# Performance work log

Hardware: AMD Instinct MI355X
Metric: run time of the kernel (lower is better)

The kernel has to match this reference:

```python
import jax, jax.numpy as jnp
import numpy as np

H = 1024
HEADS = 16
FFN = 4096
EPS = 1e-5


def _layernorm(x, g, b):
    mu = jnp.mean(x, axis=-1, keepdims=True)
    var = jnp.mean((x - mu) ** 2, axis=-1, keepdims=True)
    return (x - mu) * jax.lax.rsqrt(var + EPS) * g + b


def setup_inputs() -> dict:
    key = jax.random.key(0)
    ks = jax.random.split(key, 12)
    N, L = 2, 2048
    s = 1.0 / np.sqrt(H)
    inp = {
        "src_hidden": jax.random.normal(ks[0], (N, L, H), dtype=jnp.float32),
        "key_mask": jnp.ones((N, L), dtype=jnp.int32),
        "Wq": jax.random.normal(ks[1], (H, H), dtype=jnp.float32) * s,
        "bq": jnp.zeros((H,), dtype=jnp.float32),
        "Wk": jax.random.normal(ks[2], (H, H), dtype=jnp.float32) * s,
        "bk": jnp.zeros((H,), dtype=jnp.float32),
        "Wv": jax.random.normal(ks[3], (H, H), dtype=jnp.float32) * s,
        "bv": jnp.zeros((H,), dtype=jnp.float32),
        "Wo": jax.random.normal(ks[4], (H, H), dtype=jnp.float32) * s,
        "bo": jnp.zeros((H,), dtype=jnp.float32),
        "ln1_g": jnp.ones((H,), dtype=jnp.float32),
        "ln1_b": jnp.zeros((H,), dtype=jnp.float32),
        "W1": jax.random.normal(ks[5], (H, FFN), dtype=jnp.float32) * s,
        "b1": jnp.zeros((FFN,), dtype=jnp.float32),
        "W2": jax.random.normal(ks[6], (FFN, H), dtype=jnp.float32) * (1.0 / np.sqrt(FFN)),
        "b2": jnp.zeros((H,), dtype=jnp.float32),
        "ln2_g": jnp.ones((H,), dtype=jnp.float32),
        "ln2_b": jnp.zeros((H,), dtype=jnp.float32),
    }
    return inp


def reference(src_hidden, key_mask, Wq, bq, Wk, bk, Wv, bv, Wo, bo,
              ln1_g, ln1_b, W1, b1, W2, b2, ln2_g, ln2_b):
    N, L, _ = src_hidden.shape
    d = H // HEADS
    # projections -> (N, heads, L, d)
    q = (src_hidden @ Wq + bq).reshape(N, L, HEADS, d).transpose(0, 2, 1, 3)
    k = (src_hidden @ Wk + bk).reshape(N, L, HEADS, d).transpose(0, 2, 1, 3)
    v = (src_hidden @ Wv + bv).reshape(N, L, HEADS, d).transpose(0, 2, 1, 3)
    # faithful quirk: Q/=sqrt(H) and K/=sqrt(H)  =>  scores scaled by 1/H
    sims = jnp.einsum('bhid,bhjd->bhij', q, k) / H  # (N, heads, L, L)
    mask = key_mask[:, None, None, :] != 0          # (N,1,1,L), masked=False
    sims = jnp.where(mask, sims, -jnp.inf)
    attn = jax.nn.softmax(sims, axis=-1)
    ctx = jnp.einsum('bhij,bhjd->bhid', attn, v)
    concats = ctx.transpose(0, 2, 1, 3).reshape(N, L, H)
    mhsa = concats @ Wo + bo
    # residual + LN1
    x = _layernorm(mhsa + src_hidden, ln1_g, ln1_b)
    # FFN (dropout=0 / eval) + residual + LN2
    ffn = jax.nn.relu(x @ W1 + b1) @ W2 + b2
    out = _layernorm(ffn + x, ln2_g, ln2_b)
    return out
```

## Files before the change

### kernel.cpp

```cpp
#include <hip/hip_runtime.h>
#include <math.h>

#define Hd   1024
#define SEQL 2048
#define NB   2
#define NHEADS 16
#define FFND 4096
#define ROWS 4096
#define QKVLD 3072

typedef __attribute__((ext_vector_type(8))) short short8;
typedef __attribute__((ext_vector_type(4))) float f32x4;

__device__ __forceinline__ unsigned short f2bf(float f) {
  union { float f; unsigned int u; } v; v.f = f;
  return (unsigned short)((v.u + 0x7fffu + ((v.u >> 16) & 1u)) >> 16);
}
__device__ __forceinline__ unsigned short f2bf_fast(float f) {
  union { float f; unsigned int u; } v; v.f = f;
  return (unsigned short)((v.u + 0x8000u) >> 16);
}
__device__ __forceinline__ float bf2f(unsigned short u) {
  union { unsigned int u; float f; } v; v.u = (unsigned int)u << 16;
  return v.f;
}

__device__ __forceinline__ void gl_lds16(const unsigned short* g,
                                         unsigned short* l) {
  __builtin_amdgcn_global_load_lds(
      (const __attribute__((address_space(1))) void*)g,
      (__attribute__((address_space(3))) void*)l, 16, 0, 0);
}

__global__ __launch_bounds__(256) void convert_bf16(
    const float* __restrict__ in, unsigned short* __restrict__ out) {
  const int i = (blockIdx.x * 256 + threadIdx.x) * 4;
  float4 x = *(const float4*)&in[i];
  ushort4 o;
  o.x = f2bf(x.x); o.y = f2bf(x.y); o.z = f2bf(x.z); o.w = f2bf(x.w);
  *(ushort4*)&out[i] = o;
}

__global__ __launch_bounds__(256) void convert_transpose(
    const float* __restrict__ W, int ld,
    unsigned short* __restrict__ Wt, int ldt) {
  __shared__ float T[64][65];
  const int t = threadIdx.x;
  const int c0 = blockIdx.x * 64, r0 = blockIdx.y * 64;
#pragma unroll
  for (int p = 0; p < 4; ++p) {
    const int lin = t + p * 256;
    const int r = lin >> 4, c4 = (lin & 15) * 4;
    float4 x = *(const float4*)&W[(size_t)(r0 + r) * ld + c0 + c4];
    T[r][c4 + 0] = x.x; T[r][c4 + 1] = x.y;
    T[r][c4 + 2] = x.z; T[r][c4 + 3] = x.w;
  }
  __syncthreads();
#pragma unroll
  for (int p = 0; p < 2; ++p) {
    const int lin = t + p * 256;
    const int oc = lin >> 3, ch = (lin & 7) * 8;
    union { unsigned short u[8]; uint4 v; } x;
#pragma unroll
    for (int i = 0; i < 8; ++i) x.u[i] = f2bf(T[ch + i][oc]);
    *(uint4*)&Wt[(size_t)(c0 + oc) * ldt + r0 + ch] = x.v;
  }
}

__global__ __launch_bounds__(256) void convert_transpose4(
    const float* __restrict__ W0, const float* __restrict__ W1,
    const float* __restrict__ W2, const float* __restrict__ W3,
    unsigned short* __restrict__ T0, unsigned short* __restrict__ T1,
    unsigned short* __restrict__ T2, unsigned short* __restrict__ T3) {
  __shared__ float T[64][65];
  const float* W = (blockIdx.z == 0) ? W0 : (blockIdx.z == 1) ? W1
                 : (blockIdx.z == 2) ? W2 : W3;
  unsigned short* Wt = (blockIdx.z == 0) ? T0 : (blockIdx.z == 1) ? T1
                     : (blockIdx.z == 2) ? T2 : T3;
  const int t = threadIdx.x;
  const int c0 = blockIdx.x * 64, r0 = blockIdx.y * 64;
#pragma unroll
  for (int p = 0; p < 4; ++p) {
    const int lin = t + p * 256;
    const int r = lin >> 4, c4 = (lin & 15) * 4;
    float4 x = *(const float4*)&W[(size_t)(r0 + r) * Hd + c0 + c4];
    T[r][c4 + 0] = x.x; T[r][c4 + 1] = x.y;
    T[r][c4 + 2] = x.z; T[r][c4 + 3] = x.w;
  }
  __syncthreads();
#pragma unroll
  for (int p = 0; p < 2; ++p) {
    const int lin = t + p * 256;
    const int oc = lin >> 3, ch = (lin & 7) * 8;
    union { unsigned short u[8]; uint4 v; } x;
#pragma unroll
    for (int i = 0; i < 8; ++i) x.u[i] = f2bf(T[ch + i][oc]);
    *(uint4*)&Wt[(size_t)(c0 + oc) * Hd + r0 + ch] = x.v;
  }
}

__global__ __launch_bounds__(256) void concat3(
    const float* __restrict__ a, const float* __restrict__ b,
    const float* __restrict__ c, float* __restrict__ o) {
  const int i = blockIdx.x * 256 + threadIdx.x;
  o[i] = (i < 1024) ? a[i] : (i < 2048 ? b[i - 1024] : c[i - 2048]);
}

__global__ __launch_bounds__(256) void transpose_v(
    const unsigned short* __restrict__ v, unsigned short* __restrict__ vt) {
  __shared__ unsigned short T[64][72];
  const int t = threadIdx.x;
  const int s0 = (blockIdx.x & 31) * 64;
  const int bh = blockIdx.x >> 5;
  const int b = bh >> 4, h = bh & 15;
#pragma unroll
  for (int p = 0; p < 2; ++p) {
    const int lin = t + p * 256;
    const int r = lin >> 3, c8 = (lin & 7) * 8;
    *(uint4*)&T[r][c8] =
        *(const uint4*)&v[(size_t)(b * SEQL + s0 + r) * QKVLD + h * 64 + c8];
  }
  __syncthreads();
#pragma unroll
  for (int p = 0; p < 2; ++p) {
    const int lin = t + p * 256;
    const int d = lin >> 3, c8 = (lin & 7) * 8;
    union { unsigned short u[8]; uint4 v4; } x;
#pragma unroll
    for (int i = 0; i < 8; ++i) x.u[i] = T[c8 + i][d];
    *(uint4*)&vt[(size_t)(bh * 64 + d) * SEQL + s0 + c8] = x.v4;
  }
}

template <int BN, int MODE, int OUTBF>
__global__ __launch_bounds__(256, (BN == 128 ? 3 : 4)) void gemm_bt(
    const unsigned short* __restrict__ A, int lda,
    const unsigned short* __restrict__ Bt, int ldb,
    const float* __restrict__ bias,
    void* __restrict__ Cv, int ldc, int K) {
  constexpr int NI = (BN == 128) ? 4 : 2;
  __shared__ unsigned short As[128 * 32];
  __shared__ unsigned short Bs[BN * 32];
  const int t = threadIdx.x;
  const int wave = t >> 6, lane = t & 63;
  const int l16 = lane & 15, quad = lane >> 4;
  const int m0 = blockIdx.y * 128, n0 = blockIdx.x * BN;
  const int wm = (wave >> 1) * 64, wn = (wave & 1) * (BN / 2);
  const int srow = wave * 16 + (lane >> 2);
  const int scol = (lane & 3) * 8;

  f32x4 acc[4][NI];
#pragma unroll
  for (int i = 0; i < 4; ++i)
#pragma unroll
    for (int j = 0; j < NI; ++j) acc[i][j] = (f32x4){0.f, 0.f, 0.f, 0.f};

  const unsigned short* Ap0 = &A[(size_t)(m0 + srow) * lda + scol];
  const unsigned short* Ap1 = &A[(size_t)(m0 + 64 + srow) * lda + scol];
  const unsigned short* Bp0 = &Bt[(size_t)(n0 + srow) * ldb + scol];
  const unsigned short* Bp1 =
      (BN == 128) ? &Bt[(size_t)(n0 + 64 + srow) * ldb + scol] : Bp0;
  unsigned short* lA0 = &As[(wave * 16) * 32];
  unsigned short* lA1 = &As[(64 + wave * 16) * 32];
  unsigned short* lB0 = &Bs[(wave * 16) * 32];
  unsigned short* lB1 = (BN == 128) ? &Bs[(64 + wave * 16) * 32] : lB0;

  for (int k0 = 0; k0 < K; k0 += 32) {
    gl_lds16(Ap0 + k0, lA0);
    gl_lds16(Ap1 + k0, lA1);
    gl_lds16(Bp0 + k0, lB0);
    if (BN == 128) gl_lds16(Bp1 + k0, lB1);
    __syncthreads();

    short8 af[4], bfr[NI];
#pragma unroll
    for (int mi = 0; mi < 4; ++mi)
      af[mi] = *(const short8*)&As[(wm + mi * 16 + l16) * 32 + quad * 8];
#pragma unroll
    for (int ni = 0; ni < NI; ++ni)
      bfr[ni] = *(const short8*)&Bs[(wn + ni * 16 + l16) * 32 + quad * 8];
#pragma unroll
    for (int mi = 0; mi < 4; ++mi)
#pragma unroll
      for (int ni = 0; ni < NI; ++ni)
        acc[mi][ni] = __builtin_amdgcn_mfma_f32_16x16x32_bf16(
            af[mi], bfr[ni], acc[mi][ni], 0, 0, 0);
    __syncthreads();
  }

#pragma unroll
  for (int mi = 0; mi < 4; ++mi) {
#pragma unroll
    for (int ni = 0; ni < NI; ++ni) {
      const int col = n0 + wn + ni * 16 + l16;
      const float bv = (MODE == 2) ? 0.0f : bias[col];
#pragma unroll
      for (int r = 0; r < 4; ++r) {
        const int row = m0 + wm + mi * 16 + quad * 4 + r;
        float v = acc[mi][ni][r] + bv;
        if (MODE == 1) v = fmaxf(v, 0.0f);
        if (OUTBF) {
          ((unsigned short*)Cv)[(size_t)row * ldc + col] = f2bf_fast(v);
        } else {
          float* Cf = (float*)Cv;
          if (MODE == 2) Cf[(size_t)row * ldc + col] += v;
          else           Cf[(size_t)row * ldc + col] = v;
        }
      }
    }
  }
}

template <int MODE>
__global__ __launch_bounds__(512, 2) void gemm256(
    const unsigned short* __restrict__ A, int lda,
    const unsigned short* __restrict__ Bt, int ldb,
    const float* __restrict__ bias,
    unsigned short* __restrict__ C, int ldc, int K) {
  __shared__ unsigned short As[2][256 * 64];
  __shared__ unsigned short Bs[2][256 * 64];
  const int t = threadIdx.x;
  const int wave = t >> 6, lane = t & 63;
  const int l16 = lane & 15, quad = lane >> 4;
  const int m0 = blockIdx.y * 256, n0 = blockIdx.x * 256;
  const int wm = (wave >> 2) * 128, wn = (wave & 3) * 64;

  const int srow = t >> 3;
  const int scol = 8 * ((t & 7) ^ ((t >> 3) & 7));
  const unsigned short* Ab = &A[(size_t)(m0 + srow) * lda + scol];
  const unsigned short* Bb = &Bt[(size_t)(n0 + srow) * ldb + scol];

  auto stgA = [&](int buf, int kt, int h) {
    const unsigned short* g = Ab + (size_t)(h * 128) * lda + kt * 64;
    unsigned short* l = &As[buf][h * 8192 + wave * 512];
    gl_lds16(g, l);
    gl_lds16(g + (size_t)64 * lda, l + 4096);
  };
  auto stgB = [&](int buf, int kt, int h) {
    const unsigned short* g = Bb + (size_t)(h * 128) * ldb + kt * 64;
    unsigned short* l = &Bs[buf][h * 8192 + wave * 512];
    gl_lds16(g, l);
    gl_lds16(g + (size_t)64 * ldb, l + 4096);
  };

  f32x4 acc[8][4];
#pragma unroll
  for (int i = 0; i < 8; ++i)
#pragma unroll
    for (int j = 0; j < 4; ++j) acc[i][j] = (f32x4){0.f, 0.f, 0.f, 0.f};

  const int NT = K >> 6;

  stgA(0, 0, 0); stgA(0, 0, 1);
  stgB(0, 0, 0); stgB(0, 0, 1);
  if (NT > 1) {
    stgB(1, 1, 0); stgB(1, 1, 1);
    asm volatile("s_waitcnt vmcnt(4)" ::: "memory");
  } else {
    asm volatile("s_waitcnt vmcnt(0)" ::: "memory");
  }
  __builtin_amdgcn_s_barrier();

  short8 bq[4];
  for (int tk = 0; tk < NT; ++tk) {
    const int cb = tk & 1, nb = cb ^ 1;
    short8 af[4];

#pragma unroll
    for (int mi = 0; mi < 4; ++mi) {
      const int r = wm + mi * 16 + l16;
      af[mi] = *(const short8*)&As[cb][r * 64 + ((quad * 8) ^ ((r & 7) * 8))];
    }
#pragma unroll
    for (int ni = 0; ni < 4; ++ni) {
      const int r = wn + ni * 16 + l16;
      bq[ni] = *(const short8*)&Bs[cb][r * 64 + ((quad * 8) ^ ((r & 7) * 8))];
    }
    if (tk + 1 < NT) stgA(nb, tk + 1, 0);
    __builtin_amdgcn_sched_barrier(0);
    __builtin_amdgcn_s_barrier();
    asm volatile("s_waitcnt lgkmcnt(0)" ::: "memory");
    __builtin_amdgcn_sched_barrier(0);
    __builtin_amdgcn_s_setprio(1);
#pragma unroll
    for (int mi = 0; mi < 4; ++mi)
#pragma unroll
      for (int ni = 0; ni < 4; ++ni)
        acc[mi][ni] = __builtin_amdgcn_mfma_f32_16x16x32_bf16(
            af[mi], bq[ni], acc[mi][ni], 0, 0, 0);
    __builtin_amdgcn_s_setprio(0);
    __builtin_amdgcn_s_barrier();

#pragma unroll
    for (int mi = 0; mi < 4; ++mi) {
      const int r = wm + 64 + mi * 16 + l16;
      af[mi] = *(const short8*)&As[cb][r * 64 + ((quad * 8) ^ ((r & 7) * 8))];
    }
    if (tk + 1 < NT) stgA(nb, tk + 1, 1);
    __builtin_amdgcn_sched_barrier(0);
    __builtin_amdgcn_s_barrier();
    asm volatile("s_waitcnt lgkmcnt(0)" ::: "memory");
    __builtin_amdgcn_sched_barrier(0);
    __builtin_amdgcn_s_setprio(1);
#pragma unroll
    for (int mi = 0; mi < 4; ++mi)
#pragma unroll
      for (int ni = 0; ni < 4; ++ni)
        acc[4 + mi][ni] = __builtin_amdgcn_mfma_f32_16x16x32_bf16(
            af[mi], bq[ni], acc[4 + mi][ni], 0, 0, 0);
    __builtin_amdgcn_s_setprio(0);
    __builtin_amdgcn_s_barrier();

#pragma unroll
    for (int mi = 0; mi < 4; ++mi) {
      const int r = wm + mi * 16 + l16;
      af[mi] = *(const short8*)&As[cb][r * 64 + ((32 + quad * 8) ^ ((r & 7) * 8))];
    }
#pragma unroll
    for (int ni = 0; ni < 4; ++ni) {
      const int r = wn + ni * 16 + l16;
      bq[ni] = *(const short8*)&Bs[cb][r * 64 + ((32 + quad * 8) ^ ((r & 7) * 8))];
    }
    __builtin_amdgcn_sched_barrier(0);
    __builtin_amdgcn_s_barrier();
    asm volatile("s_waitcnt lgkmcnt(0)" ::: "memory");
    __builtin_amdgcn_sched_barrier(0);
    __builtin_amdgcn_s_setprio(1);
#pragma unroll
    for (int mi = 0; mi < 4; ++mi)
#pragma unroll
      for (int ni = 0; ni < 4; ++ni)
        acc[mi][ni] = __builtin_amdgcn_mfma_f32_16x16x32_bf16(
            af[mi], bq[ni], acc[mi][ni], 0, 0, 0);
    __builtin_amdgcn_s_setprio(0);
    __builtin_amdgcn_s_barrier();

#pragma unroll
    for (int mi = 0; mi < 4; ++mi) {
      const int r = wm + 64 + mi * 16 + l16;
      af[mi] = *(const short8*)&As[cb][r * 64 + ((32 + quad * 8) ^ ((r & 7) * 8))];
    }
    if (tk + 2 < NT) { stgB(cb, tk + 2, 0); stgB(cb, tk + 2, 1); }
    __builtin_amdgcn_sched_barrier(0);
    __builtin_amdgcn_s_barrier();
    asm volatile("s_waitcnt lgkmcnt(0)" ::: "memory");
    __builtin_amdgcn_sched_barrier(0);
    __builtin_amdgcn_s_setprio(1);
#pragma unroll
    for (int mi = 0; mi < 4; ++mi)
#pragma unroll
      for (int ni = 0; ni < 4; ++ni)
        acc[4 + mi][ni] = __builtin_amdgcn_mfma_f32_16x16x32_bf16(
            af[mi], bq[ni], acc[4 + mi][ni], 0, 0, 0);
    __builtin_amdgcn_s_setprio(0);
    if (tk + 2 < NT) {
      asm volatile("s_waitcnt vmcnt(4)" ::: "memory");
    } else if (tk + 1 < NT) {
      asm volatile("s_waitcnt vmcnt(0)" ::: "memory");
    }
    __builtin_amdgcn_s_barrier();
  }

#pragma unroll
  for (int mi = 0; mi < 8; ++mi) {
#pragma unroll
    for (int ni = 0; ni < 4; ++ni) {
      const int col = n0 + wn + ni * 16 + l16;
      const float bv = bias[col];
#pragma unroll
      for (int r = 0; r < 4; ++r) {
        const int row = m0 + wm + mi * 16 + quad * 4 + r;
        float v = acc[mi][ni][r] + bv;
        if (MODE == 1) v = fmaxf(v, 0.0f);
        C[(size_t)row * ldc + col] = f2bf_fast(v);
      }
    }
  }
}

__global__ __launch_bounds__(256, 5) void attn_mfma(
    const unsigned short* __restrict__ Q,
    const unsigned short* __restrict__ K,
    const unsigned short* __restrict__ Vt,
    const int* __restrict__ mask,
    unsigned short* __restrict__ Op,
    float* __restrict__ ls) {
  __shared__ unsigned short Qs[64 * 72];
  __shared__ unsigned short Ks[64 * 72];
  __shared__ unsigned short Vs[64 * 72];
  unsigned short* Ps = Qs;

  const int t = threadIdx.x;
  const int wave = t >> 6, lane = t & 63;
  const int l16 = lane & 15, quad = lane >> 4;
  const int qb = blockIdx.x & 31;
  const int h  = (blockIdx.x >> 5) & 15;
  const int b  = (blockIdx.x >> 9) & 1;
  const int jh = blockIdx.x >> 10;
  const int q0 = qb * 64;
  const int bh = b * NHEADS + h;
  const int jbeg = jh * (SEQL / 2), jend = jbeg + SEQL / 2;
  const float NEGINF = -__builtin_inff();

  const int lr = t >> 3, lc8 = (t & 7) * 8;
  const unsigned short* Kbase = &K[(size_t)(b * SEQL + lr) * QKVLD + h * 64 + lc8];
  const unsigned short* Vbase = &Vt[(size_t)(bh * 64 + lr) * SEQL + lc8];
  const size_t Krow32 = (size_t)32 * QKVLD;

#pragma unroll
  for (int p = 0; p < 2; ++p) {
    const int r = lr + p * 32;
    *(uint4*)&Qs[r * 72 + lc8] =
        *(const uint4*)&Q[(size_t)(b * SEQL + q0 + r) * QKVLD + h * 64 + lc8];
  }
  __syncthreads();
  const short8 aq0 = *(const short8*)&Qs[(wave * 16 + l16) * 72 + quad * 8];
  const short8 aq1 = *(const short8*)&Qs[(wave * 16 + l16) * 72 + 32 + quad * 8];

  float lrow[4] = {0.f, 0.f, 0.f, 0.f};
  f32x4 accO[4];
#pragma unroll
  for (int nd = 0; nd < 4; ++nd) accO[nd] = (f32x4){0.f, 0.f, 0.f, 0.f};

  uint4 kv0 = *(const uint4*)(Kbase + (size_t)jbeg * QKVLD);
  uint4 kv1 = *(const uint4*)(Kbase + (size_t)jbeg * QKVLD + Krow32);
  uint4 vv0 = *(const uint4*)(Vbase + jbeg);
  uint4 vv1 = *(const uint4*)(Vbase + jbeg + 32 * SEQL);

  for (int j0 = jbeg; j0 < jend; j0 += 64) {
    __syncthreads();
    *(uint4*)&Ks[lr * 72 + lc8] = kv0;
    *(uint4*)&Ks[(lr + 32) * 72 + lc8] = kv1;
    *(uint4*)&Vs[lr * 72 + lc8] = vv0;
    *(uint4*)&Vs[(lr + 32) * 72 + lc8] = vv1;
    __syncthreads();

    if (j0 + 64 < jend) {
      const unsigned short* kp = Kbase + (size_t)(j0 + 64) * QKVLD;
      const unsigned short* vp = Vbase + (j0 + 64);
      kv0 = *(const uint4*)(kp);
      kv1 = *(const uint4*)(kp + Krow32);
      vv0 = *(const uint4*)(vp);
      vv1 = *(const uint4*)(vp + 32 * SEQL);
    }

#pragma unroll
    for (int nt = 0; nt < 4; ++nt) {
      short8 bk0 = *(const short8*)&Ks[(nt * 16 + l16) * 72 + quad * 8];
      short8 bk1 = *(const short8*)&Ks[(nt * 16 + l16) * 72 + 32 + quad * 8];
      f32x4 z = (f32x4){0.f, 0.f, 0.f, 0.f};
      z = __builtin_amdgcn_mfma_f32_16x16x32_bf16(aq0, bk0, z, 0, 0, 0);
      z = __builtin_amdgcn_mfma_f32_16x16x32_bf16(aq1, bk1, z, 0, 0, 0);
      const bool ok = mask[b * SEQL + j0 + nt * 16 + l16] != 0;
      unsigned short pk[4];
#pragma unroll
      for (int r = 0; r < 4; ++r) {
        const float x = ok ? z[r] * (1.0f / 1024.0f) : NEGINF;
        const float p = __expf(x);
        lrow[r] += p;
        pk[r] = f2bf_fast(p);
      }
#pragma unroll
      for (int r = 0; r < 4; ++r)
        Ps[(wave * 16 + quad * 4 + r) * 72 + nt * 16 + l16] = pk[r];
    }

    short8 ap0 = *(const short8*)&Ps[(wave * 16 + l16) * 72 + quad * 8];
    short8 ap1 = *(const short8*)&Ps[(wave * 16 + l16) * 72 + 32 + quad * 8];
#pragma unroll
    for (int nd = 0; nd < 4; ++nd) {
      short8 bv0 = *(const short8*)&Vs[(nd * 16 + l16) * 72 + quad * 8];
      short8 bv1 = *(const short8*)&Vs[(nd * 16 + l16) * 72 + 32 + quad * 8];
      accO[nd] = __builtin_amdgcn_mfma_f32_16x16x32_bf16(ap0, bv0, accO[nd], 0, 0, 0);
      accO[nd] = __builtin_amdgcn_mfma_f32_16x16x32_bf16(ap1, bv1, accO[nd], 0, 0, 0);
    }
  }

#pragma unroll
  for (int r = 0; r < 4; ++r) {
#pragma unroll
    for (int off = 1; off < 16; off <<= 1)
      lrow[r] += __shfl_xor(lrow[r], off, 64);
  }
  if (l16 == 0) {
#pragma unroll
    for (int r = 0; r < 4; ++r)
      ls[((size_t)(jh * NB + b) * NHEADS + h) * SEQL + q0 + wave * 16 +
         quad * 4 + r] = lrow[r];
  }
#pragma unroll
  for (int nd = 0; nd < 4; ++nd)
#pragma unroll
    for (int r = 0; r < 4; ++r) {
      const int rowg = b * SEQL + q0 + wave * 16 + quad * 4 + r;
      Op[(size_t)jh * ROWS * Hd + (size_t)rowg * Hd + h * 64 + nd * 16 + l16] =
          f2bf_fast(accO[nd][r]);
    }
}

__global__ __launch_bounds__(256) void attn_combine(
    const unsigned short* __restrict__ Op, const float* __restrict__ ls,
    unsigned short* __restrict__ ctxb) {
  const int row = blockIdx.x;
  const int b = row >> 11, q = row & (SEQL - 1);
  const int t = threadIdx.x;
  const int c0 = t * 4, h = t >> 4;
  const float l0 = ls[((size_t)(b)*NHEADS + h) * SEQL + q];
  const float l1 = ls[((size_t)(NB + b) * NHEADS + h) * SEQL + q];
  const float inv = 1.0f / (l0 + l1);
  ushort4 a = *(const ushort4*)&Op[(size_t)row * Hd + c0];
  ushort4 c = *(const ushort4*)&Op[(size_t)ROWS * Hd + (size_t)row * Hd + c0];
  ushort4 o;
  o.x = f2bf_fast((bf2f(a.x) + bf2f(c.x)) * inv);
  o.y = f2bf_fast((bf2f(a.y) + bf2f(c.y)) * inv);
  o.z = f2bf_fast((bf2f(a.z) + bf2f(c.z)) * inv);
  o.w = f2bf_fast((bf2f(a.w) + bf2f(c.w)) * inv);
  *(ushort4*)&ctxb[(size_t)row * Hd + c0] = o;
}

template <int ABF>
__global__ __launch_bounds__(256) void add_ln_kernel(
    const void* Av, const float* R,
    const float* __restrict__ gamma, const float* __restrict__ beta,
    float* out, unsigned short* outb) {
  const int row = blockIdx.x;
  const int t = threadIdx.x;
  const size_t baser = (size_t)row * Hd;

  float a0, a1, a2, a3;
  if (ABF) {
    ushort4 a = *(const ushort4*)&((const unsigned short*)Av)[baser + t * 4];
    a0 = bf2f(a.x); a1 = bf2f(a.y); a2 = bf2f(a.z); a3 = bf2f(a.w);
  } else {
    float4 a = *(const float4*)&((const float*)Av)[baser + t * 4];
    a0 = a.x; a1 = a.y; a2 = a.z; a3 = a.w;
  }
  float4 r = *(const float4*)&R[baser + t * 4];
  float x0 = a0 + r.x, x1 = a1 + r.y, x2 = a2 + r.z, x3 = a3 + r.w;
  float s  = x0 + x1 + x2 + x3;
  float ss = x0 * x0 + x1 * x1 + x2 * x2 + x3 * x3;

#pragma unroll
  for (int off = 32; off > 0; off >>= 1) {
    s  += __shfl_down(s, off, 64);
    ss += __shfl_down(ss, off, 64);
  }

  __shared__ float rs[4], rss[4];
  __shared__ float sh_mean, sh_rstd;
  if ((t & 63) == 0) { rs[t >> 6] = s; rss[t >> 6] = ss; }
  __syncthreads();
  if (t == 0) {
    const float S  = rs[0] + rs[1] + rs[2] + rs[3];
    const float SS = rss[0] + rss[1] + rss[2] + rss[3];
    const float mean = S * (1.0f / Hd);
    const float var  = SS * (1.0f / Hd) - mean * mean;
    sh_mean = mean;
    sh_rstd = rsqrtf(var + 1e-5f);
  }
  __syncthreads();
  const float mean = sh_mean, rstd = sh_rstd;

  float4 gm = *(const float4*)&gamma[t * 4];
  float4 bt = *(const float4*)&beta[t * 4];
  float4 o;
  o.x = (x0 - mean) * rstd * gm.x + bt.x;
  o.y = (x1 - mean) * rstd * gm.y + bt.y;
  o.z = (x2 - mean) * rstd * gm.z + bt.z;
  o.w = (x3 - mean) * rstd * gm.w + bt.w;
  *(float4*)&out[baser + t * 4] = o;
  if (outb) {
    ushort4 ob;
    ob.x = f2bf(o.x); ob.y = f2bf(o.y); ob.z = f2bf(o.z); ob.w = f2bf(o.w);
    *(ushort4*)&outb[baser + t * 4] = ob;
  }
}

extern "C" void kernel_launch(void* const* d_in, const int* in_sizes, int n_in,
                              void* d_out, int out_size, void* d_ws, size_t ws_size,
                              hipStream_t stream) {
  const float* src  = (const float*)d_in[0];
  const int*   kmsk = (const int*)  d_in[1];
  const float* Wq   = (const float*)d_in[2];
  const float* bq   = (const float*)d_in[3];
  const float* Wk   = (const float*)d_in[4];
  const float* bk   = (const float*)d_in[5];
  const float* Wv   = (const float*)d_in[6];
  const float* bv   = (const float*)d_in[7];
  const float* Wo   = (const float*)d_in[8];
  const float* bo   = (const float*)d_in[9];
  const float* ln1g = (const float*)d_in[10];
  const float* ln1b = (const float*)d_in[11];
  const float* W1   = (const float*)d_in[12];
  const float* b1   = (const float*)d_in[13];
  const float* W2   = (const float*)d_in[14];
  const float* b2   = (const float*)d_in[15];
  const float* ln2g = (const float*)d_in[16];
  const float* ln2b = (const float*)d_in[17];

  char* w8 = (char*)d_ws;
  char* o8 = (char*)d_out;
  const size_t MB = 1024 * 1024;
  unsigned short* srcb  = (unsigned short*)(w8 + 0 * MB);
  unsigned short* WqkvT = (unsigned short*)(w8 + 8 * MB);
  float*          bqkv  = (float*)(w8 + 14 * MB);
  unsigned short* qkv   = (unsigned short*)(w8 + 16 * MB);
  unsigned short* vt    = (unsigned short*)(w8 + 40 * MB);
  unsigned short* Opart = (unsigned short*)(w8 + 0 * MB);
  float*          ls    = (float*)(o8 + 8 * MB);
  unsigned short* WoT   = (unsigned short*)(o8 + 9 * MB);
  unsigned short* ctxb  = (unsigned short*)d_out;
  float*          mhsa  = (float*)(w8 + 16 * MB);
  float*          x1    = (float*)d_out;
  unsigned short* x1b   = (unsigned short*)(w8 + 8 * MB);
  unsigned short* W1T   = (unsigned short*)(w8 + 0 * MB);
  unsigned short* hb    = (unsigned short*)(w8 + 16 * MB);
  unsigned short* W2T   = (unsigned short*)(w8 + 0 * MB);
  unsigned short* f2b   = (unsigned short*)(w8 + 8 * MB);

  dim3 blk(256);
  dim3 blk8(512);

  convert_bf16<<<ROWS * Hd / 1024, blk, 0, stream>>>(src, srcb);
  convert_transpose4<<<dim3(16, 16, 4), blk, 0, stream>>>(
      Wq, Wk, Wv, Wo, WqkvT, WqkvT + 1024 * 1024, WqkvT + 2 * 1024 * 1024, WoT);
  concat3<<<12, blk, 0, stream>>>(bq, bk, bv, bqkv);

  gemm256<0><<<dim3(QKVLD / 256, ROWS / 256), blk8, 0, stream>>>(
      srcb, Hd, WqkvT, Hd, bqkv, qkv, QKVLD, Hd);

  transpose_v<<<1024, blk, 0, stream>>>(qkv + 2048, vt);
  attn_mfma<<<2048, blk, 0, stream>>>(qkv, qkv + 1024, vt, kmsk, Opart, ls);
  attn_combine<<<ROWS, blk, 0, stream>>>(Opart, ls, ctxb);

  gemm_bt<64, 0, 0><<<dim3(Hd / 64, ROWS / 128), blk, 0, stream>>>(
      ctxb, Hd, WoT, Hd, bo, mhsa, Hd, Hd);

  add_ln_kernel<0><<<ROWS, blk, 0, stream>>>(mhsa, src, ln1g, ln1b, x1, x1b);

  convert_transpose<<<dim3(64, 16), blk, 0, stream>>>(W1, FFND, W1T, Hd);
  gemm256<1><<<dim3(FFND / 256, ROWS / 256), blk8, 0, stream>>>(
      x1b, Hd, W1T, Hd, b1, hb, FFND, Hd);
  convert_transpose<<<dim3(16, 64), blk, 0, stream>>>(W2, Hd, W2T, FFND);
  gemm_bt<64, 0, 1><<<dim3(Hd / 64, ROWS / 128), blk, 0, stream>>>(
      hb, FFND, W2T, FFND, b2, f2b, Hd, FFND);

  add_ln_kernel<1><<<ROWS, blk, 0, stream>>>(f2b, x1, ln2g, ln2b,
                                             (float*)d_out, nullptr);
}
```

Baseline: 404.2 us.

## Drop attention split-K, change GEMM tile widths, loosen gemm256 barriers

Attention no longer splits the key range into two halves. Each block now processes all 2048 keys and normalises its output directly, which removes the partial-output buffer and the attn_combine kernel. The Wo and W2 GEMMs switch to 128-wide tiles, and gemm256 drops its explicit sched_barrier and lgkmcnt(0) waits around the LDS reads and barriers. The trade-off is half as many attention blocks, each doing twice the serial work, which lowers occupancy; removing the explicit LDS waits also relies on the compiler inserting the correct waits itself.

New measurement: 423.2 us. +4.7%, slower.

```diff
diff --git a/kernel.cpp b/kernel.cpp
--- a/kernel.cpp
+++ b/kernel.cpp
@@ -277,10 +277,7 @@
       bq[ni] = *(const short8*)&Bs[cb][r * 64 + ((quad * 8) ^ ((r & 7) * 8))];
     }
     if (tk + 1 < NT) stgA(nb, tk + 1, 0);
-    __builtin_amdgcn_sched_barrier(0);
-    __builtin_amdgcn_s_barrier();
-    asm volatile("s_waitcnt lgkmcnt(0)" ::: "memory");
-    __builtin_amdgcn_sched_barrier(0);
+    __builtin_amdgcn_s_barrier();
     __builtin_amdgcn_s_setprio(1);
 #pragma unroll
     for (int mi = 0; mi < 4; ++mi)
@@ -297,10 +294,7 @@
       af[mi] = *(const short8*)&As[cb][r * 64 + ((quad * 8) ^ ((r & 7) * 8))];
     }
     if (tk + 1 < NT) stgA(nb, tk + 1, 1);
-    __builtin_amdgcn_sched_barrier(0);
-    __builtin_amdgcn_s_barrier();
-    asm volatile("s_waitcnt lgkmcnt(0)" ::: "memory");
-    __builtin_amdgcn_sched_barrier(0);
+    __builtin_amdgcn_s_barrier();
     __builtin_amdgcn_s_setprio(1);
 #pragma unroll
     for (int mi = 0; mi < 4; ++mi)
@@ -321,10 +315,7 @@
       const int r = wn + ni * 16 + l16;
       bq[ni] = *(const short8*)&Bs[cb][r * 64 + ((32 + quad * 8) ^ ((r & 7) * 8))];
     }
-    __builtin_amdgcn_sched_barrier(0);
-    __builtin_amdgcn_s_barrier();
-    asm volatile("s_waitcnt lgkmcnt(0)" ::: "memory");
-    __builtin_amdgcn_sched_barrier(0);
+    __builtin_amdgcn_s_barrier();
     __builtin_amdgcn_s_setprio(1);
 #pragma unroll
     for (int mi = 0; mi < 4; ++mi)
@@ -341,10 +332,7 @@
       af[mi] = *(const short8*)&As[cb][r * 64 + ((32 + quad * 8) ^ ((r & 7) * 8))];
     }
     if (tk + 2 < NT) { stgB(cb, tk + 2, 0); stgB(cb, tk + 2, 1); }
-    __builtin_amdgcn_sched_barrier(0);
-    __builtin_amdgcn_s_barrier();
-    asm volatile("s_waitcnt lgkmcnt(0)" ::: "memory");
-    __builtin_amdgcn_sched_barrier(0);
+    __builtin_amdgcn_s_barrier();
     __builtin_amdgcn_s_setprio(1);
 #pragma unroll
     for (int mi = 0; mi < 4; ++mi)
@@ -383,8 +371,7 @@
     const unsigned short* __restrict__ K,
     const unsigned short* __restrict__ Vt,
     const int* __restrict__ mask,
-    unsigned short* __restrict__ Op,
-    float* __restrict__ ls) {
+    unsigned short* __restrict__ ctxb) {
   __shared__ unsigned short Qs[64 * 72];
   __shared__ unsigned short Ks[64 * 72];
   __shared__ unsigned short Vs[64 * 72];
@@ -395,11 +382,9 @@
   const int l16 = lane & 15, quad = lane >> 4;
   const int qb = blockIdx.x & 31;
   const int h  = (blockIdx.x >> 5) & 15;
-  const int b  = (blockIdx.x >> 9) & 1;
-  const int jh = blockIdx.x >> 10;
+  const int b  = blockIdx.x >> 9;
   const int q0 = qb * 64;
   const int bh = b * NHEADS + h;
-  const int jbeg = jh * (SEQL / 2), jend = jbeg + SEQL / 2;
   const float NEGINF = -__builtin_inff();
 
   const int lr = t >> 3, lc8 = (t & 7) * 8;
@@ -422,12 +407,12 @@
 #pragma unroll
   for (int nd = 0; nd < 4; ++nd) accO[nd] = (f32x4){0.f, 0.f, 0.f, 0.f};
 
-  uint4 kv0 = *(const uint4*)(Kbase + (size_t)jbeg * QKVLD);
-  uint4 kv1 = *(const uint4*)(Kbase + (size_t)jbeg * QKVLD + Krow32);
-  uint4 vv0 = *(const uint4*)(Vbase + jbeg);
-  uint4 vv1 = *(const uint4*)(Vbase + jbeg + 32 * SEQL);
-
-  for (int j0 = jbeg; j0 < jend; j0 += 64) {
+  uint4 kv0 = *(const uint4*)(Kbase);
+  uint4 kv1 = *(const uint4*)(Kbase + Krow32);
+  uint4 vv0 = *(const uint4*)(Vbase);
+  uint4 vv1 = *(const uint4*)(Vbase + 32 * SEQL);
+
+  for (int j0 = 0; j0 < SEQL; j0 += 64) {
     __syncthreads();
     *(uint4*)&Ks[lr * 72 + lc8] = kv0;
     *(uint4*)&Ks[(lr + 32) * 72 + lc8] = kv1;
@@ -435,7 +420,7 @@
     *(uint4*)&Vs[(lr + 32) * 72 + lc8] = vv1;
     __syncthreads();
 
-    if (j0 + 64 < jend) {
+    if (j0 + 64 < SEQL) {
       const unsigned short* kp = Kbase + (size_t)(j0 + 64) * QKVLD;
       const unsigned short* vp = Vbase + (j0 + 64);
       kv0 = *(const uint4*)(kp);
@@ -482,40 +467,18 @@
     for (int off = 1; off < 16; off <<= 1)
       lrow[r] += __shfl_xor(lrow[r], off, 64);
   }
-  if (l16 == 0) {
-#pragma unroll
-    for (int r = 0; r < 4; ++r)
-      ls[((size_t)(jh * NB + b) * NHEADS + h) * SEQL + q0 + wave * 16 +
-         quad * 4 + r] = lrow[r];
-  }
+  float inv[4];
+#pragma unroll
+  for (int r = 0; r < 4; ++r) inv[r] = 1.0f / lrow[r];
+
 #pragma unroll
   for (int nd = 0; nd < 4; ++nd)
 #pragma unroll
     for (int r = 0; r < 4; ++r) {
       const int rowg = b * SEQL + q0 + wave * 16 + quad * 4 + r;
-      Op[(size_t)jh * ROWS * Hd + (size_t)rowg * Hd + h * 64 + nd * 16 + l16] =
-          f2bf_fast(accO[nd][r]);
-    }
-}
-
-__global__ __launch_bounds__(256) void attn_combine(
-    const unsigned short* __restrict__ Op, const float* __restrict__ ls,
-    unsigned short* __restrict__ ctxb) {
-  const int row = blockIdx.x;
-  const int b = row >> 11, q = row & (SEQL - 1);
-  const int t = threadIdx.x;
-  const int c0 = t * 4, h = t >> 4;
-  const float l0 = ls[((size_t)(b)*NHEADS + h) * SEQL + q];
-  const float l1 = ls[((size_t)(NB + b) * NHEADS + h) * SEQL + q];
-  const float inv = 1.0f / (l0 + l1);
-  ushort4 a = *(const ushort4*)&Op[(size_t)row * Hd + c0];
-  ushort4 c = *(const ushort4*)&Op[(size_t)ROWS * Hd + (size_t)row * Hd + c0];
-  ushort4 o;
-  o.x = f2bf_fast((bf2f(a.x) + bf2f(c.x)) * inv);
-  o.y = f2bf_fast((bf2f(a.y) + bf2f(c.y)) * inv);
-  o.z = f2bf_fast((bf2f(a.z) + bf2f(c.z)) * inv);
-  o.w = f2bf_fast((bf2f(a.w) + bf2f(c.w)) * inv);
-  *(ushort4*)&ctxb[(size_t)row * Hd + c0] = o;
+      ctxb[(size_t)rowg * Hd + h * 64 + nd * 16 + l16] =
+          f2bf_fast(accO[nd][r] * inv[r]);
+    }
 }
 
 template <int ABF>
@@ -606,8 +569,6 @@
   float*          bqkv  = (float*)(w8 + 14 * MB);
   unsigned short* qkv   = (unsigned short*)(w8 + 16 * MB);
   unsigned short* vt    = (unsigned short*)(w8 + 40 * MB);
-  unsigned short* Opart = (unsigned short*)(w8 + 0 * MB);
-  float*          ls    = (float*)(o8 + 8 * MB);
   unsigned short* WoT   = (unsigned short*)(o8 + 9 * MB);
   unsigned short* ctxb  = (unsigned short*)d_out;
   float*          mhsa  = (float*)(w8 + 16 * MB);
@@ -630,10 +591,9 @@
       srcb, Hd, WqkvT, Hd, bqkv, qkv, QKVLD, Hd);
 
   transpose_v<<<1024, blk, 0, stream>>>(qkv + 2048, vt);
-  attn_mfma<<<2048, blk, 0, stream>>>(qkv, qkv + 1024, vt, kmsk, Opart, ls);
-  attn_combine<<<ROWS, blk, 0, stream>>>(Opart, ls, ctxb);
-
-  gemm_bt<64, 0, 0><<<dim3(Hd / 64, ROWS / 128), blk, 0, stream>>>(
+  attn_mfma<<<1024, blk, 0, stream>>>(qkv, qkv + 1024, vt, kmsk, ctxb);
+
+  gemm_bt<128, 0, 0><<<dim3(Hd / 128, ROWS / 128), blk, 0, stream>>>(
       ctxb, Hd, WoT, Hd, bo, mhsa, Hd, Hd);
 
   add_ln_kernel<0><<<ROWS, blk, 0, stream>>>(mhsa, src, ln1g, ln1b, x1, x1b);
@@ -642,7 +602,7 @@
   gemm256<1><<<dim3(FFND / 256, ROWS / 256), blk8, 0, stream>>>(
       x1b, Hd, W1T, Hd, b1, hb, FFND, Hd);
   convert_transpose<<<dim3(16, 64), blk, 0, stream>>>(W2, Hd, W2T, FFND);
-  gemm_bt<64, 0, 1><<<dim3(Hd / 64, ROWS / 128), blk, 0, stream>>>(
+  gemm_bt<128, 0, 1><<<dim3(Hd / 128, ROWS / 128), blk, 0, stream>>>(
       hb, FFND, W2T, FFND, b2, f2b, Hd, FFND);
 
   add_ln_kernel<1><<<ROWS, blk, 0, stream>>>(f2b, x1, ln2g, ln2b,
```
